# Kernel optimization log

Measured on AMD Instinct MI355X. Metric: run time of the kernel, lower is better.

## Reference

```python
import jax, jax.numpy as jnp
import numpy as np

N = 4_000_000
G = 512          # input grid extent per axis
GP = G // 2      # parent (output) grid extent
SENT = jnp.iinfo(jnp.int32).max  # sort-stable sentinel for padded unique slots


def setup_inputs() -> dict:
    key = jax.random.key(0)
    k1, k2 = jax.random.split(key)
    coords = jax.random.randint(k1, (N, 4), 0, G, dtype=jnp.int32)
    coords = coords.at[:, 0].set(0)  # single batch
    feats = jax.random.normal(k2, (N, 1), dtype=jnp.float32)
    return {"coords": coords, "feats": feats}


def reference(coords, feats):
    # Sparse conv3d, kernel 2x2x2, stride 2, identity (8,1,8) weights ==
    # space-to-depth fold: out[parent, offset_id] = sum of inputs at that
    # offset inside the 2x2x2 block (sum handles duplicate coords like conv).
    b = coords[:, 0]
    xyz = coords[:, 1:]
    parent = xyz >> 1                     # [N,3] output voxel coords
    off = xyz & 1                         # [N,3] position within block
    offset_id = off[:, 0] * 4 + off[:, 1] * 2 + off[:, 2]  # lexicographic (dx,dy,dz)

    # Linearize parent voxel (batch-major) for dedup.
    key_lin = ((b * GP + parent[:, 0]) * GP + parent[:, 1]) * GP + parent[:, 2]

    # Fixed-size (jit-friendly) unique: sorted, padded at end with SENT.
    ukeys = jnp.unique(key_lin, size=N, fill_value=SENT)
    idx = jnp.searchsorted(ukeys, key_lin)  # row in output for each input point

    out_feats = jnp.zeros((N, 8), feats.dtype).at[idx, offset_id].add(feats[:, 0])

    # Decode output coords; mark padded rows with -1.
    kz = ukeys % GP
    ky = (ukeys // GP) % GP
    kx = (ukeys // (GP * GP)) % GP
    kb = ukeys // (GP * GP * GP)
    out_coords = jnp.stack([kb, kx, ky, kz], axis=1).astype(jnp.int32)
    valid = (ukeys != SENT)[:, None]
    out_coords = jnp.where(valid, out_coords, -1)
    return out_coords, out_feats
```

## Files before the change

kernel.cpp:

```cpp
#include <hip/hip_runtime.h>
#include <stdint.h>


static constexpr int      PTS_A  = 2048;
static constexpr int      PTS_B  = 4096;
static constexpr int      NB_A   = 64;
static constexpr int      SHARDS = 8;
static constexpr int      SEGS   = NB_A * SHARDS;
static constexpr uint32_t CAP_A  = 12288;
static constexpr int      BPS_B  = CAP_A / PTS_B;
static constexpr int      NB_B   = 256;
static constexpr int      NBKT   = NB_A * NB_B;
static constexpr uint32_t CAP_B  = 384;

__device__ __forceinline__ uint32_t make_pk(int4 c) {
    uint32_t key = ((((uint32_t)c.x << 8 | (uint32_t)(c.y >> 1)) << 8 |
                     (uint32_t)(c.z >> 1)) << 8) | (uint32_t)(c.w >> 1);
    uint32_t off = (uint32_t)(c.y & 1) * 4u + (uint32_t)(c.z & 1) * 2u + (uint32_t)(c.w & 1);
    return (key << 3) | off;
}

__device__ __forceinline__ uint32_t wave_incl_scan(uint32_t v, uint32_t lane) {
    #pragma unroll
    for (int d = 1; d < 64; d <<= 1) {
        uint32_t u = __shfl_up(v, d, 64);
        if (lane >= (uint32_t)d) v += u;
    }
    return v;
}

__global__ __launch_bounds__(256) void passA_kernel(const int4* __restrict__ coords,
                                                    const float* __restrict__ feats,
                                                    uint32_t* __restrict__ cursorA,
                                                    uint2* __restrict__ bufA, int n) {
    __shared__ uint32_t hist[NB_A], scx[NB_A], gbase[NB_A];
    __shared__ uint2 stage[PTS_A];
    int t = threadIdx.x, blk = blockIdx.x;
    int base = blk * PTS_A;
    if (t < NB_A) hist[t] = 0;
    __syncthreads();
    uint32_t pk[8]; float f[8]; uint16_t loc[8]; uint8_t bk[8];
    if (base + PTS_A <= n) {
        #pragma unroll
        for (int j = 0; j < 8; j++) {
            int i = base + j * 256 + t;
            pk[j] = make_pk(coords[i]);
            f[j] = feats[i];
            bk[j] = (uint8_t)(pk[j] >> 21);
            loc[j] = (uint16_t)atomicAdd(&hist[bk[j]], 1u);
        }
    } else {
        #pragma unroll
        for (int j = 0; j < 8; j++) {
            int i = base + j * 256 + t;
            if (i < n) {
                pk[j] = make_pk(coords[i]);
                f[j] = feats[i];
                bk[j] = (uint8_t)(pk[j] >> 21);
                loc[j] = (uint16_t)atomicAdd(&hist[bk[j]], 1u);
            } else pk[j] = 0xFFFFFFFFu;
        }
    }
    __syncthreads();
    if (t < NB_A) {
        uint32_t h = hist[t];
        uint32_t incl = wave_incl_scan(h, (uint32_t)t);
        uint32_t excl = incl - h;
        uint32_t shard = (uint32_t)t * SHARDS + (uint32_t)(blk & (SHARDS - 1));
        uint32_t old = atomicAdd(&cursorA[shard * 16], h);
        gbase[t] = shard * CAP_A + old;
        scx[t] = excl;
    }
    __syncthreads();
    #pragma unroll
    for (int j = 0; j < 8; j++)
        if (pk[j] != 0xFFFFFFFFu)
            stage[scx[bk[j]] + loc[j]] = make_uint2(pk[j], __float_as_uint(f[j]));
    int total = (base + PTS_A <= n) ? PTS_A : (n - base);
    __syncthreads();
    for (int s = t; s < total; s += 256) {
        uint2 p = stage[s];
        uint32_t b = p.x >> 21;
        bufA[gbase[b] + ((uint32_t)s - scx[b])] = p;
    }
}

__global__ __launch_bounds__(256) void passB_kernel(const uint2* __restrict__ bufA,
                                                    const uint32_t* __restrict__ cursorA,
                                                    uint32_t* __restrict__ cursorB,
                                                    uint2* __restrict__ bufB) {
    __shared__ uint32_t hist[NB_B], scx[NB_B], gold[NB_B];
    __shared__ uint32_t wsum[4];
    __shared__ uint2 stage[PTS_B];
    int t = threadIdx.x, g = blockIdx.x;
    int sIdx = g / BPS_B, sub = g % BPS_B;
    uint32_t segBase = (uint32_t)sIdx * CAP_A;
    uint32_t segCnt = cursorA[sIdx * 16];
    if (segCnt > CAP_A) segCnt = CAP_A;
    int start = sub * PTS_B;
    int cnt = (int)segCnt - start;
    if (cnt > PTS_B) cnt = PTS_B;
    if (cnt < 0) cnt = 0;
    uint32_t aBase = (uint32_t)(sIdx >> 3) * NB_B;
    hist[t] = 0;
    __syncthreads();
    uint2 pr[16]; uint16_t loc[16]; uint8_t bk[16];
    #pragma unroll
    for (int j = 0; j < 16; j++) {
        int i = j * 256 + t;
        if (i < cnt) {
            pr[j] = bufA[segBase + start + i];
            bk[j] = (uint8_t)((pr[j].x >> 13) & 255u);
            loc[j] = (uint16_t)atomicAdd(&hist[bk[j]], 1u);
        }
    }
    __syncthreads();
    {
        uint32_t lane = (uint32_t)t & 63u, wave = (uint32_t)t >> 6;
        uint32_t h = hist[t];
        uint32_t incl = wave_incl_scan(h, lane);
        if (lane == 63u) wsum[wave] = incl;
        __syncthreads();
        uint32_t add = 0;
        #pragma unroll
        for (uint32_t w = 0; w < 4; w++) if (w < wave) add += wsum[w];
        incl += add;
        uint32_t excl = incl - h;
        gold[t] = atomicAdd(&cursorB[aBase + (uint32_t)t], h);
        scx[t] = excl;
    }
    __syncthreads();
    #pragma unroll
    for (int j = 0; j < 16; j++) {
        int i = j * 256 + t;
        if (i < cnt) stage[scx[bk[j]] + loc[j]] = pr[j];
    }
    __syncthreads();
    for (int s = t; s < cnt; s += 256) {
        uint2 p = stage[s];
        uint32_t b = (p.x >> 13) & 255u;
        uint32_t pos = gold[b] + ((uint32_t)s - scx[b]);
        if (pos < CAP_B) bufB[(size_t)(aBase + b) * CAP_B + pos] = p;
    }
}

__global__ __launch_bounds__(256) void count_kernel(const uint2* __restrict__ bufB,
                                                    const uint32_t* __restrict__ cursorB,
                                                    uint32_t* __restrict__ ucount,
                                                    uint32_t* __restrict__ bitmapG) {
    __shared__ uint32_t bm[32];
    int t = threadIdx.x, b = blockIdx.x;
    uint32_t cnt = cursorB[b]; if (cnt > CAP_B) cnt = CAP_B;
    if (t < 32) bm[t] = 0;
    __syncthreads();
    uint32_t base = (uint32_t)b * CAP_B;
    for (uint32_t i = t; i < cnt; i += 256) {
        uint32_t pk = bufB[base + i].x;
        atomicOr(&bm[(pk >> 8) & 31u], 1u << ((pk >> 3) & 31u));
    }
    __syncthreads();
    if (t < 32) {
        uint32_t w = bm[t];
        bitmapG[(uint32_t)b * 32u + (uint32_t)t] = w;
        uint32_t s = (uint32_t)__popc(w);
        #pragma unroll
        for (int d = 1; d < 32; d <<= 1) s += __shfl_xor(s, d, 64);
        if (t == 0) ucount[b] = s;
    }
}

__global__ __launch_bounds__(1024) void scanU_kernel(const uint32_t* __restrict__ ucount,
                                                     uint32_t* __restrict__ baseRank,
                                                     uint32_t* __restrict__ totalOut) {
    __shared__ uint32_t s[1024];
    int t = threadIdx.x;
    uint32_t v[16]; uint32_t sum = 0;
    #pragma unroll
    for (int j = 0; j < 16; j++) { v[j] = ucount[t * 16 + j]; sum += v[j]; }
    s[t] = sum;
    __syncthreads();
    for (int d = 1; d < 1024; d <<= 1) {
        uint32_t x = (t >= d) ? s[t - d] : 0u;
        __syncthreads();
        s[t] += x;
        __syncthreads();
    }
    uint32_t run = s[t] - sum;
    #pragma unroll
    for (int j = 0; j < 16; j++) { baseRank[t * 16 + j] = run; run += v[j]; }
    if (t == 1023) *totalOut = s[1023];
}

__global__ __launch_bounds__(256) void fold_tail_kernel(const uint2* __restrict__ bufB,
                                                        const uint32_t* __restrict__ cursorB,
                                                        const uint32_t* __restrict__ bitmapG,
                                                        const uint32_t* __restrict__ baseRank,
                                                        const uint32_t* __restrict__ totalPtr,
                                                        float4* __restrict__ outCoords,
                                                        float4* __restrict__ outFeats2, int n) {
    __shared__ float acc[9216];
    __shared__ uint32_t bm[32], wp[32];
    __shared__ uint16_t keylist[1024];
    int t = threadIdx.x, b = blockIdx.x;
    uint32_t cnt = cursorB[b]; if (cnt > CAP_B) cnt = CAP_B;
    float4* acc4 = (float4*)acc;
    float4 z4 = make_float4(0.f, 0.f, 0.f, 0.f);
    for (int i = t; i < 2304; i += 256) acc4[i] = z4;
    if (t < 32) bm[t] = bitmapG[(uint32_t)b * 32u + (uint32_t)t];
    __syncthreads();
    uint32_t base = (uint32_t)b * CAP_B;
    for (uint32_t i = t; i < cnt; i += 256) {
        uint2 p = bufB[base + i];
        atomicAdd(&acc[((p.x >> 3) & 1023u) * 9u + (p.x & 7u)], __uint_as_float(p.y));
    }
    if (t < 32) {
        uint32_t s = (uint32_t)__popc(bm[t]);
        #pragma unroll
        for (int d = 1; d < 32; d <<= 1) {
            uint32_t u = __shfl_up(s, d, 64);
            if ((uint32_t)t >= (uint32_t)d) s += u;
        }
        wp[t] = s;
    }
    __syncthreads();
    for (int k = t; k < 1024; k += 256) {
        uint32_t w = (uint32_t)k >> 5, bit = (uint32_t)k & 31u, word = bm[w];
        if ((word >> bit) & 1u) {
            uint32_t lr = wp[w] - (uint32_t)__popc(word) + (uint32_t)__popc(word & ((1u << bit) - 1u));
            keylist[lr] = (uint16_t)k;
        }
    }
    __syncthreads();
    int ucnt = (int)wp[31];
    uint32_t rbase = baseRank[b];
    for (int u = t; u < ucnt; u += 256) {
        uint32_t k = keylist[u];
        uint32_t rank = rbase + (uint32_t)u;
        uint32_t key = ((uint32_t)b << 10) | k;
        outCoords[rank] = make_float4((float)(key >> 24), (float)((key >> 16) & 255u),
                                      (float)((key >> 8) & 255u), (float)(key & 255u));
        float4 lo, hi;
        lo.x = acc[k * 9 + 0]; lo.y = acc[k * 9 + 1]; lo.z = acc[k * 9 + 2]; lo.w = acc[k * 9 + 3];
        hi.x = acc[k * 9 + 4]; hi.y = acc[k * 9 + 5]; hi.z = acc[k * 9 + 6]; hi.w = acc[k * 9 + 7];
        outFeats2[(size_t)rank * 2] = lo;
        outFeats2[(size_t)rank * 2 + 1] = hi;
    }
    uint32_t U = *totalPtr;
    uint32_t rows = ((uint32_t)n > U) ? (uint32_t)n - U : 0u;
    uint32_t per = (rows + (uint32_t)gridDim.x - 1u) / (uint32_t)gridDim.x;
    uint32_t s0 = U + (uint32_t)b * per;
    uint32_t s1 = s0 + per; if (s1 > (uint32_t)n) s1 = (uint32_t)n;
    for (uint32_t i = s0 + (uint32_t)t; i < s1; i += 256u) {
        outCoords[i] = make_float4(-1.f, -1.f, -1.f, -1.f);
        outFeats2[(size_t)i * 2] = z4;
        outFeats2[(size_t)i * 2 + 1] = z4;
    }
}

static constexpr uint32_t NKEYS  = 1u << 24;
static constexpr uint32_t NWORDS = 1u << 19;
static constexpr int SCAN_BLOCKS = 512;

__global__ void zero_u4(uint4* __restrict__ p, int count) {
    int i = blockIdx.x * blockDim.x + threadIdx.x;
    int stride = gridDim.x * blockDim.x;
    uint4 z = {0u, 0u, 0u, 0u};
    for (; i < count; i += stride) p[i] = z;
}

__global__ void bytemark_kernel(const int4* __restrict__ coords, uint8_t* __restrict__ bytemap,
                                uint32_t* __restrict__ pkey, int n) {
    int i = blockIdx.x * blockDim.x + threadIdx.x;
    if (i >= n) return;
    uint32_t pk = make_pk(coords[i]);
    bytemap[pk >> 3] = 1;
    pkey[i] = pk;
}

__global__ void build_scan1_kernel(const uint4* __restrict__ bytemap4, uint4* __restrict__ bitmap4,
                                   uint32_t* __restrict__ blockSums) {
    __shared__ uint32_t red[256];
    int t = threadIdx.x;
    int base = blockIdx.x * 256 + t;
    uint4 wb;
    uint32_t* wordOut = (uint32_t*)&wb;
    uint32_t sum = 0;
    #pragma unroll
    for (int j = 0; j < 4; j++) {
        uint4 lo = bytemap4[base * 8 + j * 2];
        uint4 hi = bytemap4[base * 8 + j * 2 + 1];
        const uint32_t* cl = (const uint32_t*)&lo;
        const uint32_t* ch = (const uint32_t*)&hi;
        uint32_t bits = 0;
        #pragma unroll
        for (int k = 0; k < 4; k++)
            bits |= (((cl[k] & 0x01010101u) * 0x10204080u) >> 28) << (4 * k);
        #pragma unroll
        for (int k = 0; k < 4; k++)
            bits |= (((ch[k] & 0x01010101u) * 0x10204080u) >> 28) << (16 + 4 * k);
        wordOut[j] = bits;
        sum += (uint32_t)__popc(bits);
    }
    bitmap4[base] = wb;
    red[t] = sum;
    __syncthreads();
    for (int d = 128; d > 0; d >>= 1) {
        if (t < d) red[t] += red[t + d];
        __syncthreads();
    }
    if (t == 0) blockSums[blockIdx.x] = red[0];
}

__global__ void scan2_kernel(const uint32_t* __restrict__ blockSums, uint32_t* __restrict__ blockOffsets,
                             uint32_t* __restrict__ totalOut) {
    __shared__ uint32_t s[SCAN_BLOCKS];
    int t = threadIdx.x;
    uint32_t v = blockSums[t];
    s[t] = v;
    __syncthreads();
    for (int d = 1; d < SCAN_BLOCKS; d <<= 1) {
        uint32_t x = (t >= d) ? s[t - d] : 0u;
        __syncthreads();
        s[t] += x;
        __syncthreads();
    }
    blockOffsets[t] = s[t] - v;
    if (t == SCAN_BLOCKS - 1) *totalOut = s[t];
}

__global__ void scan3_kernel(const uint4* __restrict__ bitmap4, const uint32_t* __restrict__ blockOffsets,
                             uint4* __restrict__ wordPrefix4) {
    __shared__ uint32_t s[256];
    int t = threadIdx.x;
    int gi = blockIdx.x * 256 + t;
    uint4 w = bitmap4[gi];
    uint32_t p0 = __popc(w.x), p1 = __popc(w.y), p2 = __popc(w.z), p3 = __popc(w.w);
    uint32_t tot = p0 + p1 + p2 + p3;
    s[t] = tot;
    __syncthreads();
    for (int d = 1; d < 256; d <<= 1) {
        uint32_t x = (t >= d) ? s[t - d] : 0u;
        __syncthreads();
        s[t] += x;
        __syncthreads();
    }
    uint32_t excl = s[t] - tot + blockOffsets[blockIdx.x];
    uint4 wp;
    wp.x = excl; wp.y = wp.x + p0; wp.z = wp.y + p1; wp.w = wp.z + p2;
    wordPrefix4[gi] = wp;
}

__global__ void decode_kernel(const uint4* __restrict__ bitmap4, const uint4* __restrict__ wordPrefix4,
                              float4* __restrict__ outCoords) {
    int gi = blockIdx.x * blockDim.x + threadIdx.x;
    if (gi >= (int)(NWORDS / 4)) return;
    uint4 w = bitmap4[gi];
    uint4 wp = wordPrefix4[gi];
    uint32_t words[4] = {w.x, w.y, w.z, w.w};
    uint32_t prefs[4] = {wp.x, wp.y, wp.z, wp.w};
    #pragma unroll
    for (int j = 0; j < 4; j++) {
        uint32_t word = words[j];
        uint32_t rank = prefs[j];
        uint32_t baseKey = ((uint32_t)gi * 4u + (uint32_t)j) * 32u;
        while (word) {
            uint32_t bb = (uint32_t)__ffs(word) - 1u;
            word &= word - 1u;
            uint32_t key = baseKey + bb;
            outCoords[rank++] = make_float4((float)(key >> 24), (float)((key >> 16) & 255u),
                                            (float)((key >> 8) & 255u), (float)(key & 255u));
        }
    }
}

__global__ void tail_fill_kernel(float4* __restrict__ outCoords, float4* __restrict__ outFeats2,
                                 const uint32_t* __restrict__ totalPtr, int n) {
    int i = blockIdx.x * blockDim.x + threadIdx.x;
    if (i >= n) return;
    uint32_t U = *totalPtr;
    if ((uint32_t)i < U) return;
    outCoords[i] = make_float4(-1.f, -1.f, -1.f, -1.f);
    float4 z = make_float4(0.f, 0.f, 0.f, 0.f);
    outFeats2[(size_t)i * 2] = z;
    outFeats2[(size_t)i * 2 + 1] = z;
}

__global__ void scatter_pk_kernel(const uint32_t* __restrict__ pkey, const float* __restrict__ feats,
                                  const uint32_t* __restrict__ bitmap, const uint32_t* __restrict__ wordPrefix,
                                  float* __restrict__ outFeats, int n) {
    int i = blockIdx.x * blockDim.x + threadIdx.x;
    if (i >= n) return;
    uint32_t pk = pkey[i];
    uint32_t key = pk >> 3, off = pk & 7u;
    uint32_t w = key >> 5, bb = key & 31u;
    uint32_t idx = wordPrefix[w] + (uint32_t)__popc(bitmap[w] & ((1u << bb) - 1u));
    atomicAdd(outFeats + (size_t)idx * 8u + off, feats[i]);
}

extern "C" void kernel_launch(void* const* d_in, const int* in_sizes, int n_in,
                              void* d_out, int out_size, void* d_ws, size_t ws_size,
                              hipStream_t stream) {
    const int4* coords = (const int4*)d_in[0];
    const float* feats = (const float*)d_in[1];
    int n = in_sizes[0] / 4;

    float* out = (float*)d_out;
    float4* outCoords = (float4*)out;
    float* outFeats = out + (size_t)n * 4;
    float4* outFeats2 = (float4*)outFeats;

    uint8_t* ws = (uint8_t*)d_ws;
    int ptBlocks = (n + 255) / 256;

    uint32_t* cursorA  = (uint32_t*)ws;
    uint32_t* cursorB  = (uint32_t*)(ws + (32u << 10));
    uint32_t* ucountP  = (uint32_t*)(ws + (128u << 10));
    uint32_t* baseRank = (uint32_t*)(ws + (192u << 10));
    uint32_t* totalU   = (uint32_t*)(ws + (256u << 10));
    uint32_t* bitmapG  = (uint32_t*)(ws + (512u << 10));
    uint2* bufA = (uint2*)(ws + (4u << 20));
    uint2* bufB = (uint2*)(ws + (4u << 20) + (size_t)SEGS * CAP_A * 8);
    size_t need2 = (4u << 20) + (size_t)SEGS * CAP_A * 8 + (size_t)NBKT * CAP_B * 8;

    if (ws_size >= need2) {
        hipMemsetAsync(ws, 0, (96u << 10), stream);
        passA_kernel<<<(n + PTS_A - 1) / PTS_A, 256, 0, stream>>>(coords, feats, cursorA, bufA, n);
        passB_kernel<<<SEGS * BPS_B, 256, 0, stream>>>(bufA, cursorA, cursorB, bufB);
        count_kernel<<<NBKT, 256, 0, stream>>>(bufB, cursorB, ucountP, bitmapG);
        scanU_kernel<<<1, 1024, 0, stream>>>(ucountP, baseRank, totalU);
        fold_tail_kernel<<<NBKT, 256, 0, stream>>>(bufB, cursorB, bitmapG, baseRank, totalU,
                                                   outCoords, outFeats2, n);
        return;
    }

    uint32_t* bitmap       = (uint32_t*)ws;
    uint32_t* wordPrefix   = (uint32_t*)(ws + (size_t)NWORDS * 4);
    uint32_t* blockSums    = (uint32_t*)(ws + (size_t)NWORDS * 8);
    uint32_t* blockOffsets = blockSums + SCAN_BLOCKS;
    uint32_t* totalPtr     = blockOffsets + SCAN_BLOCKS;
    uint8_t*  bytemap      = ws + (size_t)NWORDS * 8 + 8192;
    uint32_t* pkey         = (uint32_t*)(bytemap + NKEYS);

    zero_u4<<<2048, 256, 0, stream>>>((uint4*)outFeats, (int)(((size_t)n * 8) / 4));
    zero_u4<<<1024, 256, 0, stream>>>((uint4*)bytemap, (int)(NKEYS / 16));
    bytemark_kernel<<<ptBlocks, 256, 0, stream>>>(coords, bytemap, pkey, n);
    build_scan1_kernel<<<SCAN_BLOCKS, 256, 0, stream>>>((const uint4*)bytemap, (uint4*)bitmap, blockSums);
    scan2_kernel<<<1, SCAN_BLOCKS, 0, stream>>>(blockSums, blockOffsets, totalPtr);
    scan3_kernel<<<SCAN_BLOCKS, 256, 0, stream>>>((const uint4*)bitmap, blockOffsets, (uint4*)wordPrefix);
    decode_kernel<<<(int)(NWORDS / 4 + 255) / 256, 256, 0, stream>>>(
        (const uint4*)bitmap, (const uint4*)wordPrefix, outCoords);
    tail_fill_kernel<<<ptBlocks, 256, 0, stream>>>(outCoords, outFeats2, totalPtr, n);
    scatter_pk_kernel<<<ptBlocks, 256, 0, stream>>>(pkey, feats, bitmap, wordPrefix, outFeats, n);
}
```

Baseline: 350.4 us.

## Fuse count and scan into cooperative kernel, split bucket keys/values, sparse acc zeroing

Replaces the per-bucket count kernel and the single-block scan with one cooperative kernel of 1024 blocks. Each block handles 16 buckets, and grid syncs do the global prefix over block sums. The bucket buffer becomes separate key and value arrays, so the count pass reads only keys. The fold kernel now loads its points up front and zeroes only the accumulator rows of occupied keys instead of the whole shared array. The intent is to cut launch count, count-pass traffic and shared-memory zeroing, at the cost of cooperative-launch grid syncs.

```diff
diff --git a/kernel.cpp b/kernel.cpp
--- a/kernel.cpp
+++ b/kernel.cpp
@@ -1,5 +1,8 @@
 #include <hip/hip_runtime.h>
+#include <hip/hip_cooperative_groups.h>
 #include <stdint.h>
+
+namespace cg = cooperative_groups;
 
 
 static constexpr int      PTS_A  = 2048;
@@ -12,6 +15,8 @@
 static constexpr int      NB_B   = 256;
 static constexpr int      NBKT   = NB_A * NB_B;
 static constexpr uint32_t CAP_B  = 384;
+static constexpr int      CS_BLOCKS   = 1024;
+static constexpr int      BKT_PER_CS  = NBKT / CS_BLOCKS;
 
 __device__ __forceinline__ uint32_t make_pk(int4 c) {
     uint32_t key = ((((uint32_t)c.x << 8 | (uint32_t)(c.y >> 1)) << 8 |
@@ -88,7 +93,8 @@
 __global__ __launch_bounds__(256) void passB_kernel(const uint2* __restrict__ bufA,
                                                     const uint32_t* __restrict__ cursorA,
                                                     uint32_t* __restrict__ cursorB,
-                                                    uint2* __restrict__ bufB) {
+                                                    uint32_t* __restrict__ bufBk,
+                                                    float* __restrict__ bufBv) {
     __shared__ uint32_t hist[NB_B], scx[NB_B], gold[NB_B];
     __shared__ uint32_t wsum[4];
     __shared__ uint2 stage[PTS_B];
@@ -140,58 +146,91 @@
         uint2 p = stage[s];
         uint32_t b = (p.x >> 13) & 255u;
         uint32_t pos = gold[b] + ((uint32_t)s - scx[b]);
-        if (pos < CAP_B) bufB[(size_t)(aBase + b) * CAP_B + pos] = p;
-    }
-}
-
-__global__ __launch_bounds__(256) void count_kernel(const uint2* __restrict__ bufB,
-                                                    const uint32_t* __restrict__ cursorB,
-                                                    uint32_t* __restrict__ ucount,
-                                                    uint32_t* __restrict__ bitmapG) {
-    __shared__ uint32_t bm[32];
-    int t = threadIdx.x, b = blockIdx.x;
-    uint32_t cnt = cursorB[b]; if (cnt > CAP_B) cnt = CAP_B;
-    if (t < 32) bm[t] = 0;
-    __syncthreads();
-    uint32_t base = (uint32_t)b * CAP_B;
-    for (uint32_t i = t; i < cnt; i += 256) {
-        uint32_t pk = bufB[base + i].x;
-        atomicOr(&bm[(pk >> 8) & 31u], 1u << ((pk >> 3) & 31u));
-    }
-    __syncthreads();
-    if (t < 32) {
-        uint32_t w = bm[t];
-        bitmapG[(uint32_t)b * 32u + (uint32_t)t] = w;
-        uint32_t s = (uint32_t)__popc(w);
-        #pragma unroll
-        for (int d = 1; d < 32; d <<= 1) s += __shfl_xor(s, d, 64);
-        if (t == 0) ucount[b] = s;
-    }
-}
-
-__global__ __launch_bounds__(1024) void scanU_kernel(const uint32_t* __restrict__ ucount,
-                                                     uint32_t* __restrict__ baseRank,
-                                                     uint32_t* __restrict__ totalOut) {
-    __shared__ uint32_t s[1024];
-    int t = threadIdx.x;
-    uint32_t v[16]; uint32_t sum = 0;
-    #pragma unroll
-    for (int j = 0; j < 16; j++) { v[j] = ucount[t * 16 + j]; sum += v[j]; }
-    s[t] = sum;
-    __syncthreads();
-    for (int d = 1; d < 1024; d <<= 1) {
-        uint32_t x = (t >= d) ? s[t - d] : 0u;
-        __syncthreads();
-        s[t] += x;
-        __syncthreads();
-    }
-    uint32_t run = s[t] - sum;
-    #pragma unroll
-    for (int j = 0; j < 16; j++) { baseRank[t * 16 + j] = run; run += v[j]; }
-    if (t == 1023) *totalOut = s[1023];
-}
-
-__global__ __launch_bounds__(256) void fold_tail_kernel(const uint2* __restrict__ bufB,
+        if (pos < CAP_B) {
+            uint32_t o = (aBase + b) * CAP_B + pos;
+            bufBk[o] = p.x;
+            bufBv[o] = __uint_as_float(p.y);
+        }
+    }
+}
+
+__global__ __launch_bounds__(256) void count_scan_kernel(
+        const uint32_t* __restrict__ bufBk, const uint32_t* __restrict__ cursorB,
+        uint32_t* __restrict__ bitmapG, uint32_t* __restrict__ blockSum,
+        uint32_t* __restrict__ baseRank, uint32_t* __restrict__ totalOut) {
+    __shared__ uint32_t bm[BKT_PER_CS * 32];
+    __shared__ uint32_t cshift[BKT_PER_CS + 1];
+    __shared__ uint32_t ucnt_s[BKT_PER_CS];
+    __shared__ uint32_t wsumS[4];
+    int t = threadIdx.x, g = blockIdx.x;
+    uint32_t b0 = (uint32_t)g * BKT_PER_CS;
+    for (int i = t; i < BKT_PER_CS * 32; i += 256) bm[i] = 0;
+    if (t < BKT_PER_CS) {
+        uint32_t c = cursorB[b0 + (uint32_t)t]; if (c > CAP_B) c = CAP_B;
+        ucnt_s[t] = c;
+    }
+    __syncthreads();
+    if (t == 0) {
+        uint32_t r = 0;
+        #pragma unroll
+        for (int j = 0; j < BKT_PER_CS; j++) { cshift[j] = r; r += ucnt_s[j]; }
+        cshift[BKT_PER_CS] = r;
+    }
+    __syncthreads();
+    uint32_t Tp = cshift[BKT_PER_CS];
+    for (uint32_t i = t; i < Tp; i += 256u) {
+        uint32_t bb = 0;
+        if (cshift[bb + 8] <= i) bb += 8;
+        if (cshift[bb + 4] <= i) bb += 4;
+        if (cshift[bb + 2] <= i) bb += 2;
+        if (cshift[bb + 1] <= i) bb += 1;
+        uint32_t pk = bufBk[(b0 + bb) * CAP_B + (i - cshift[bb])];
+        atomicOr(&bm[(bb << 5) + ((pk >> 8) & 31u)], 1u << ((pk >> 3) & 31u));
+    }
+    __syncthreads();
+    if (t < BKT_PER_CS) {
+        uint32_t s = 0;
+        #pragma unroll
+        for (int w = 0; w < 32; w++) s += (uint32_t)__popc(bm[(t << 5) + w]);
+        ucnt_s[t] = s;
+    }
+    for (int i = t; i < BKT_PER_CS * 32; i += 256)
+        bitmapG[(size_t)b0 * 32u + (uint32_t)i] = bm[i];
+    __syncthreads();
+    if (t == 0) {
+        uint32_t s = 0;
+        #pragma unroll
+        for (int j = 0; j < BKT_PER_CS; j++) s += ucnt_s[j];
+        blockSum[g] = s;
+    }
+    cg::this_grid().sync();
+    if (g == 0) {
+        uint32_t v[4]; uint32_t s = 0;
+        #pragma unroll
+        for (int j = 0; j < 4; j++) { v[j] = blockSum[(t << 2) + j]; s += v[j]; }
+        uint32_t lane = (uint32_t)t & 63u, wave = (uint32_t)t >> 6;
+        uint32_t incl = wave_incl_scan(s, lane);
+        if (lane == 63u) wsumS[wave] = incl;
+        __syncthreads();
+        uint32_t add = 0;
+        #pragma unroll
+        for (uint32_t w = 0; w < 4; w++) if (w < wave) add += wsumS[w];
+        incl += add;
+        uint32_t run = incl - s;
+        #pragma unroll
+        for (int j = 0; j < 4; j++) { blockSum[(t << 2) + j] = run; run += v[j]; }
+        if (t == 255) *totalOut = run;
+    }
+    cg::this_grid().sync();
+    if (t == 0) {
+        uint32_t run = blockSum[g];
+        #pragma unroll
+        for (int bb = 0; bb < BKT_PER_CS; bb++) { baseRank[b0 + bb] = run; run += ucnt_s[bb]; }
+    }
+}
+
+__global__ __launch_bounds__(256) void fold_tail_kernel(const uint32_t* __restrict__ bufBk,
+                                                        const float* __restrict__ bufBv,
                                                         const uint32_t* __restrict__ cursorB,
                                                         const uint32_t* __restrict__ bitmapG,
                                                         const uint32_t* __restrict__ baseRank,
@@ -203,16 +242,14 @@
     __shared__ uint16_t keylist[1024];
     int t = threadIdx.x, b = blockIdx.x;
     uint32_t cnt = cursorB[b]; if (cnt > CAP_B) cnt = CAP_B;
-    float4* acc4 = (float4*)acc;
-    float4 z4 = make_float4(0.f, 0.f, 0.f, 0.f);
-    for (int i = t; i < 2304; i += 256) acc4[i] = z4;
+    uint32_t base = (uint32_t)b * CAP_B;
+    uint32_t k0 = 0u, k1 = 0u; float v0 = 0.f, v1 = 0.f;
+    bool h0 = (uint32_t)t < cnt;
+    bool h1 = (uint32_t)t + 256u < cnt;
+    if (h0) { k0 = bufBk[base + (uint32_t)t];        v0 = bufBv[base + (uint32_t)t]; }
+    if (h1) { k1 = bufBk[base + (uint32_t)t + 256u]; v1 = bufBv[base + (uint32_t)t + 256u]; }
     if (t < 32) bm[t] = bitmapG[(uint32_t)b * 32u + (uint32_t)t];
     __syncthreads();
-    uint32_t base = (uint32_t)b * CAP_B;
-    for (uint32_t i = t; i < cnt; i += 256) {
-        uint2 p = bufB[base + i];
-        atomicAdd(&acc[((p.x >> 3) & 1023u) * 9u + (p.x & 7u)], __uint_as_float(p.y));
-    }
     if (t < 32) {
         uint32_t s = (uint32_t)__popc(bm[t]);
         #pragma unroll
@@ -232,6 +269,15 @@
     }
     __syncthreads();
     int ucnt = (int)wp[31];
+    for (int u = t; u < ucnt; u += 256) {
+        uint32_t k = keylist[u];
+        #pragma unroll
+        for (int j = 0; j < 8; j++) acc[k * 9u + (uint32_t)j] = 0.f;
+    }
+    __syncthreads();
+    if (h0) atomicAdd(&acc[((k0 >> 3) & 1023u) * 9u + (k0 & 7u)], v0);
+    if (h1) atomicAdd(&acc[((k1 >> 3) & 1023u) * 9u + (k1 & 7u)], v1);
+    __syncthreads();
     uint32_t rbase = baseRank[b];
     for (int u = t; u < ucnt; u += 256) {
         uint32_t k = keylist[u];
@@ -245,6 +291,7 @@
         outFeats2[(size_t)rank * 2] = lo;
         outFeats2[(size_t)rank * 2 + 1] = hi;
     }
+    float4 z4 = make_float4(0.f, 0.f, 0.f, 0.f);
     uint32_t U = *totalPtr;
     uint32_t rows = ((uint32_t)n > U) ? (uint32_t)n - U : 0u;
     uint32_t per = (rows + (uint32_t)gridDim.x - 1u) / (uint32_t)gridDim.x;
@@ -414,22 +461,33 @@
 
     uint32_t* cursorA  = (uint32_t*)ws;
     uint32_t* cursorB  = (uint32_t*)(ws + (32u << 10));
-    uint32_t* ucountP  = (uint32_t*)(ws + (128u << 10));
     uint32_t* baseRank = (uint32_t*)(ws + (192u << 10));
     uint32_t* totalU   = (uint32_t*)(ws + (256u << 10));
+    uint32_t* blockSum = (uint32_t*)(ws + (260u << 10));
     uint32_t* bitmapG  = (uint32_t*)(ws + (512u << 10));
-    uint2* bufA = (uint2*)(ws + (4u << 20));
-    uint2* bufB = (uint2*)(ws + (4u << 20) + (size_t)SEGS * CAP_A * 8);
+    uint2*    bufA  = (uint2*)(ws + (4u << 20));
+    uint32_t* bufBk = (uint32_t*)(ws + (4u << 20) + (size_t)SEGS * CAP_A * 8);
+    float*    bufBv = (float*)(ws + (4u << 20) + (size_t)SEGS * CAP_A * 8
+                               + (size_t)NBKT * CAP_B * 4);
     size_t need2 = (4u << 20) + (size_t)SEGS * CAP_A * 8 + (size_t)NBKT * CAP_B * 8;
 
     if (ws_size >= need2) {
         hipMemsetAsync(ws, 0, (96u << 10), stream);
         passA_kernel<<<(n + PTS_A - 1) / PTS_A, 256, 0, stream>>>(coords, feats, cursorA, bufA, n);
-        passB_kernel<<<SEGS * BPS_B, 256, 0, stream>>>(bufA, cursorA, cursorB, bufB);
-        count_kernel<<<NBKT, 256, 0, stream>>>(bufB, cursorB, ucountP, bitmapG);
-        scanU_kernel<<<1, 1024, 0, stream>>>(ucountP, baseRank, totalU);
-        fold_tail_kernel<<<NBKT, 256, 0, stream>>>(bufB, cursorB, bitmapG, baseRank, totalU,
-                                                   outCoords, outFeats2, n);
+        passB_kernel<<<SEGS * BPS_B, 256, 0, stream>>>(bufA, cursorA, cursorB, bufBk, bufBv);
+        {
+            const uint32_t* a0 = bufBk;
+            const uint32_t* a1 = cursorB;
+            uint32_t* a2 = bitmapG;
+            uint32_t* a3 = blockSum;
+            uint32_t* a4 = baseRank;
+            uint32_t* a5 = totalU;
+            void* args[] = {&a0, &a1, &a2, &a3, &a4, &a5};
+            hipLaunchCooperativeKernel(count_scan_kernel, dim3(CS_BLOCKS), dim3(256),
+                                       args, 0, stream);
+        }
+        fold_tail_kernel<<<NBKT, 256, 0, stream>>>(bufBk, bufBv, cursorB, bitmapG, baseRank,
+                                                   totalU, outCoords, outFeats2, n);
         return;
     }
 
```

Result: slower. 541.5 us (+54.5%).
